# Performance work log

Hardware: AMD Instinct MI355X
Metric: run time of the kernel (lower is better)

The kernel has to match this reference:

```python
import jax, jax.numpy as jnp
import numpy as np

N, E, L, H, C, F, NCLASS, NGRAPH = 50000, 800000, 3, 2, 64, 128, 10, 64
NEG_SLOPE = 0.2


def setup_inputs() -> dict:
    key = jax.random.key(0)
    ks = jax.random.split(key, 8)
    x = jax.random.normal(ks[0], (N, F), dtype=jnp.float32)
    edge_index = jax.random.randint(ks[1], (2, E), 0, N, dtype=jnp.int64)
    batch = jnp.sort(jax.random.randint(ks[2], (N,), 0, NGRAPH, dtype=jnp.int64))
    s = 1.0 / np.sqrt(F)
    W = jax.random.normal(ks[3], (L, F, H * C), dtype=jnp.float32) * s
    att_src = jax.random.normal(ks[4], (L, H, C), dtype=jnp.float32) * s
    att_dst = jax.random.normal(ks[5], (L, H, C), dtype=jnp.float32) * s
    bias = jnp.zeros((L, H * C), dtype=jnp.float32)
    lin_w = jax.random.normal(ks[6], (H * C, NCLASS), dtype=jnp.float32) * s
    lin_b = jnp.zeros((NCLASS,), dtype=jnp.float32)
    return {"x": x, "edge_index": edge_index, "batch": batch, "W": W,
            "att_src": att_src, "att_dst": att_dst, "bias": bias,
            "lin_w": lin_w, "lin_b": lin_b}


def _gat_layer(x, src, dst, w, a_s, a_d, b):
    n = x.shape[0]
    h = (x @ w).reshape(n, H, C)                      # [N,H,C]
    alpha_src = jnp.sum(h * a_s, axis=-1)             # [N,H]
    alpha_dst = jnp.sum(h * a_d, axis=-1)             # [N,H]
    e = jax.nn.leaky_relu(alpha_src[src] + alpha_dst[dst], NEG_SLOPE)  # [E2,H]
    # scatter-softmax over incoming edges of each destination node
    m = jax.ops.segment_max(e, dst, num_segments=n)
    p = jnp.exp(e - m[dst])
    z = jax.ops.segment_sum(p, dst, num_segments=n)
    alpha = p / z[dst]                                # [E2,H]
    msg = h[src] * alpha[:, :, None]                  # [E2,H,C]
    out = jax.ops.segment_sum(msg, dst, num_segments=n)  # [N,H,C]
    return out.reshape(n, H * C) + b


def reference(x, edge_index, batch, W, att_src, att_dst, bias, lin_w, lin_b):
    n = x.shape[0]
    # PyG GATConv default: add self-loops
    loop = jnp.arange(n, dtype=edge_index.dtype)
    src = jnp.concatenate([edge_index[0], loop])
    dst = jnp.concatenate([edge_index[1], loop])
    for l in range(L):
        x = _gat_layer(x, src, dst, W[l], att_src[l], att_dst[l], bias[l])
        x = jax.nn.elu(x)  # activation; dropout/bn inactive (eval, use_bn=False)
    # global mean pool per graph
    sums = jax.ops.segment_sum(x, batch, num_segments=NGRAPH)
    cnt = jax.ops.segment_sum(jnp.ones((n,), x.dtype), batch, num_segments=NGRAPH)
    pooled = sums / jnp.maximum(cnt, 1.0)[:, None]    # [NGRAPH, H*C]
    logits = pooled @ lin_w + lin_b
    return jax.nn.softmax(logits, axis=1)
```

## Files before the change

kernel.cpp:

```cpp
#include <hip/hip_runtime.h>
#include <math.h>

#define NNODES 50000
#define NEDGES 800000
#define NLAYERS 3
#define NHEADS 2
#define NCH 64
#define FDIM 128
#define NCLS 10
#define NGRAPH 64
#define NEG_SLOPE 0.2f
#define GEMMB ((NNODES + 127) / 128)
#define NB 391
#define RADB 391
#define PCH 8

#define WAVE_SYNC()                      \
  do {                                   \
    __builtin_amdgcn_wave_barrier();     \
    __asm__ volatile("" ::: "memory");   \
  } while (0)

typedef __attribute__((ext_vector_type(8))) short bf16x8;
typedef __attribute__((ext_vector_type(4))) float f32x4;

__device__ __forceinline__ unsigned short f2bf(float f) {
  unsigned int u = __builtin_bit_cast(unsigned int, f);
  unsigned int r = u + 0x7FFFu + ((u >> 16) & 1u);
  return (unsigned short)(r >> 16);
}
__device__ __forceinline__ float bflo(unsigned v) {
  return __builtin_bit_cast(float, v << 16);
}
__device__ __forceinline__ float bfhi(unsigned v) {
  return __builtin_bit_cast(float, v & 0xFFFF0000u);
}

__global__ __launch_bounds__(256) void k_wprep(const float* __restrict__ W,
                                               unsigned* __restrict__ Wt,
                                               const int* __restrict__ batch,
                                               int* __restrict__ goff,
                                               float* __restrict__ gsum,
                                               int* __restrict__ bcnt,
                                               int* __restrict__ done) {
  __shared__ float Lt[128][132];
  int l = blockIdx.x;
  int t = threadIdx.x;
  if (l == NLAYERS) {
    if (t < NGRAPH) {
      int lo = 0, hi = NNODES;
      while (lo < hi) {
        int mid = (lo + hi) >> 1;
        if (batch[mid] < t) lo = mid + 1;
        else hi = mid;
      }
      goff[t] = lo;
    }
    if (t == 0) {
      goff[NGRAPH] = NNODES;
      *done = 0;
    }
    for (int i = t; i < NGRAPH * FDIM; i += 256) gsum[i] = 0.f;
    for (int i = t; i < NB; i += 256) bcnt[i] = 0;
    return;
  }
  const float* Wl = W + (size_t)l * FDIM * FDIM;
  unsigned* Wtl = Wt + (size_t)l * FDIM * FDIM / 2;
#pragma unroll
  for (int i = 0; i < 16; ++i) {
    int k = (t >> 5) + 8 * i;
    int n4 = (t & 31) * 4;
    float4 v = *(const float4*)(Wl + (size_t)k * 128 + n4);
    Lt[k][n4 + 0] = v.x;
    Lt[k][n4 + 1] = v.y;
    Lt[k][n4 + 2] = v.z;
    Lt[k][n4 + 3] = v.w;
  }
  __syncthreads();
  int n = t >> 1;
  int kh = (t & 1) * 64;
  for (int kk = 0; kk < 64; kk += 2) {
    unsigned pk = (unsigned)f2bf(Lt[kh + kk][n]) |
                  ((unsigned)f2bf(Lt[kh + kk + 1][n]) << 16);
    Wtl[n * 64 + (kh >> 1) + (kk >> 1)] = pk;
  }
}

template <bool BF16IN>
__device__ __forceinline__ void gemm_body(int blk, const void* __restrict__ Xv,
                                          const unsigned* __restrict__ Wt,
                                          const float* __restrict__ a_sL,
                                          const float* __restrict__ a_dL,
                                          unsigned* __restrict__ Hb,
                                          float* __restrict__ as_,
                                          float* __restrict__ ad_) {
  int t = threadIdx.x;
  int lane = t & 63;
  int w = t >> 6;
  int n16 = lane & 15;
  int quad = lane >> 4;
  int rowb = blk * 128 + w * 32;

  size_t rb[2];
  rb[0] = (size_t)min(rowb + n16, NNODES - 1) * 128;
  rb[1] = (size_t)min(rowb + 16 + n16, NNODES - 1) * 128;

  f32x4 acc[2][8];
#pragma unroll
  for (int mt = 0; mt < 2; ++mt)
#pragma unroll
    for (int nt = 0; nt < 8; ++nt) {
      f32x4 z = {0.f, 0.f, 0.f, 0.f};
      acc[mt][nt] = z;
    }
#pragma unroll
  for (int kk = 0; kk < 4; ++kk) {
    bf16x8 af[2];
#pragma unroll
    for (int mt = 0; mt < 2; ++mt) {
      if constexpr (BF16IN) {
        const unsigned short* xp = (const unsigned short*)Xv + rb[mt];
        af[mt] = *(const bf16x8*)(xp + kk * 32 + quad * 8);
      } else {
        const float* xp = (const float*)Xv + rb[mt];
        float4 va = *(const float4*)(xp + kk * 32 + quad * 8);
        float4 vb = *(const float4*)(xp + kk * 32 + quad * 8 + 4);
        af[mt][0] = (short)f2bf(va.x); af[mt][1] = (short)f2bf(va.y);
        af[mt][2] = (short)f2bf(va.z); af[mt][3] = (short)f2bf(va.w);
        af[mt][4] = (short)f2bf(vb.x); af[mt][5] = (short)f2bf(vb.y);
        af[mt][6] = (short)f2bf(vb.z); af[mt][7] = (short)f2bf(vb.w);
      }
    }
#pragma unroll
    for (int nt = 0; nt < 8; ++nt) {
      bf16x8 bf = *(const bf16x8*)(Wt + (size_t)(nt * 16 + n16) * 64 +
                                   kk * 16 + quad * 4);
      acc[0][nt] =
          __builtin_amdgcn_mfma_f32_16x16x32_bf16(af[0], bf, acc[0][nt], 0, 0, 0);
      acc[1][nt] =
          __builtin_amdgcn_mfma_f32_16x16x32_bf16(af[1], bf, acc[1][nt], 0, 0, 0);
    }
  }

  float asv[8], adv[8];
#pragma unroll
  for (int nt = 0; nt < 8; ++nt) {
    asv[nt] = a_sL[nt * 16 + n16];
    adv[nt] = a_dL[nt * 16 + n16];
  }
#pragma unroll
  for (int mt = 0; mt < 2; ++mt) {
#pragma unroll
    for (int r = 0; r < 4; ++r) {
      int row = rowb + mt * 16 + quad * 4 + r;
      bool ok = (row < NNODES);
      float ps0 = 0.f, pd0 = 0.f, ps1 = 0.f, pd1 = 0.f;
#pragma unroll
      for (int nt = 0; nt < 4; ++nt) {
        ps0 += acc[mt][nt][r] * asv[nt];
        pd0 += acc[mt][nt][r] * adv[nt];
        ps1 += acc[mt][nt + 4][r] * asv[nt + 4];
        pd1 += acc[mt][nt + 4][r] * adv[nt + 4];
      }
#pragma unroll
      for (int off = 1; off < 16; off <<= 1) {
        ps0 += __shfl_xor(ps0, off, 64);
        pd0 += __shfl_xor(pd0, off, 64);
        ps1 += __shfl_xor(ps1, off, 64);
        pd1 += __shfl_xor(pd1, off, 64);
      }
      if (ok && n16 == 0) {
        as_[row * 2 + 0] = ps0;
        as_[row * 2 + 1] = ps1;
        ad_[row * 2 + 0] = pd0;
        ad_[row * 2 + 1] = pd1;
      }
      if (ok) {
#pragma unroll
        for (int nt = 0; nt < 4; ++nt) {
          unsigned pk = (unsigned)f2bf(acc[mt][nt][r]) |
                        ((unsigned)f2bf(acc[mt][nt + 4][r]) << 16);
          Hb[(size_t)row * 64 + nt * 16 + n16] = pk;
        }
      }
    }
  }
}

__global__ __launch_bounds__(256) void k_gemm(
    const unsigned short* __restrict__ Xh, const unsigned* __restrict__ Wt,
    const float* __restrict__ a_sL, const float* __restrict__ a_dL,
    unsigned* __restrict__ Hb, float* __restrict__ as_,
    float* __restrict__ ad_) {
  gemm_body<true>(blockIdx.x, Xh, Wt, a_sL, a_dL, Hb, as_, ad_);
}

__global__ __launch_bounds__(256) void k_front(
    const float* __restrict__ X, const unsigned* __restrict__ Wt,
    const float* __restrict__ a_sL, const float* __restrict__ a_dL,
    unsigned* __restrict__ Hb, float* __restrict__ as_,
    float* __restrict__ ad_, const int* __restrict__ ei, int* __restrict__ bh,
    int* __restrict__ bcnt) {
  int b = blockIdx.x;
  if (b < GEMMB) {
    gemm_body<false>(b, X, Wt, a_sL, a_dL, Hb, as_, ad_);
  } else {
    __shared__ int hist[NB];
    int blk = b - GEMMB;
    int t = threadIdx.x;
    for (int i = t; i < NB; i += 256) hist[i] = 0;
    __syncthreads();
    int e0 = blk * 2048;
#pragma unroll
    for (int i = 0; i < 8; ++i) {
      int e = e0 + i * 256 + t;
      if (e < NEDGES) atomicAdd(&hist[ei[NEDGES + e] >> 7], 1);
    }
    __syncthreads();
    for (int i = t; i < NB; i += 256) {
      int c = hist[i];
      int base = c ? atomicAdd(&bcnt[i], c) : 0;
      bh[i * RADB + blk] = base;
    }
  }
}

__global__ __launch_bounds__(256) void k_passB(const int* __restrict__ ei,
                                               const int* __restrict__ bcnt,
                                               const int* __restrict__ bh,
                                               unsigned* __restrict__ ebuf,
                                               int* __restrict__ bstart) {
  __shared__ int curs[NB];
  __shared__ int ps[256];
  int blk = blockIdx.x, t = threadIdx.x;
  int x0 = (2 * t < NB) ? bcnt[2 * t] : 0;
  int x1 = (2 * t + 1 < NB) ? bcnt[2 * t + 1] : 0;
  int pair = x0 + x1;
  ps[t] = pair;
  __syncthreads();
  for (int off = 1; off < 256; off <<= 1) {
    int v = (t >= off) ? ps[t - off] : 0;
    __syncthreads();
    ps[t] += v;
    __syncthreads();
  }
  int ex = ps[t] - pair;
  if (2 * t < NB) {
    curs[2 * t] = ex + bh[(2 * t) * RADB + blk];
    if (blk == 0) bstart[2 * t] = ex;
  }
  if (2 * t + 1 < NB) {
    curs[2 * t + 1] = ex + x0 + bh[(2 * t + 1) * RADB + blk];
    if (blk == 0) bstart[2 * t + 1] = ex + x0;
  }
  if (blk == 0 && t == 0) bstart[NB] = NEDGES;
  __syncthreads();
  int e0 = blk * 2048;
#pragma unroll
  for (int i = 0; i < 8; ++i) {
    int e = e0 + i * 256 + t;
    if (e < NEDGES) {
      int s = ei[e];
      int d = ei[NEDGES + e];
      int pos = atomicAdd(&curs[d >> 7], 1);
      ebuf[pos] = ((unsigned)s << 7) | (unsigned)(d & 127);
    }
  }
}

__global__ __launch_bounds__(256) void k_passC(const unsigned* __restrict__ ebuf,
                                               const int* __restrict__ bstart,
                                               int* __restrict__ row_ptr,
                                               int* __restrict__ csr) {
  __shared__ int deg[128];
  __shared__ int scn[128];
  int b = blockIdx.x, t = threadIdx.x;
  int node0 = b * 128;
  int nn = min(128, NNODES - node0);
  int estart = bstart[b];
  int eend = bstart[b + 1];
  if (t < 128) deg[t] = 0;
  __syncthreads();
  for (int e = estart + t; e < eend; e += 256)
    atomicAdd(&deg[ebuf[e] & 127], 1);
  __syncthreads();
  if (t < 128) scn[t] = (t < nn) ? deg[t] + 1 : 0;
  __syncthreads();
  for (int off = 1; off < 128; off <<= 1) {
    int v = (t < 128 && t >= off) ? scn[t - off] : 0;
    __syncthreads();
    if (t < 128) scn[t] += v;
    __syncthreads();
  }
  int base = estart + node0;
  if (t < nn) {
    int st = base + (t ? scn[t - 1] : 0);
    row_ptr[node0 + t] = st;
    csr[st] = node0 + t;
    deg[t] = st + 1;
  }
  if (b == 0 && t == 0) row_ptr[NNODES] = NEDGES + NNODES;
  __syncthreads();
  for (int e = estart + t; e < eend; e += 256) {
    unsigned v = ebuf[e];
    int pos = atomicAdd(&deg[v & 127], 1);
    csr[pos] = (int)(v >> 7);
  }
}

__global__ __launch_bounds__(256) void k_aggregate(
    const unsigned* __restrict__ Hb, const float* __restrict__ as_,
    const float* __restrict__ ad_, const int* __restrict__ row_ptr,
    const int* __restrict__ csr, const float* __restrict__ bias,
    float* __restrict__ Xout, unsigned short* __restrict__ XoutH) {
  __shared__ float2 wb[4][64];
  __shared__ int sb[4][64];
  int wv = threadIdx.x >> 6;
  int lane = threadIdx.x & 63;
  int node = blockIdx.x * 4 + wv;
  if (node >= NNODES) return;
  int rs = row_ptr[node], re = row_ptr[node + 1];
  float2 adv = *(const float2*)&ad_[node * 2];
  const unsigned* Hl = Hb + lane;

  float z0 = 0.f, z1 = 0.f, acc0 = 0.f, acc1 = 0.f;
  for (int base = rs; base < re; base += 64) {
    int j = base + lane;
    int s = 0;
    if (j < re) s = csr[j];
    sb[wv][lane] = s;
    WAVE_SYNC();
    unsigned va[8];
#pragma unroll
    for (int u = 0; u < 8; ++u) va[u] = Hl[(size_t)sb[wv][u] * 64];
    float p0 = 0.f, p1 = 0.f;
    if (j < re) {
      float2 asv = *(const float2*)&as_[s * 2];
      float e0 = asv.x + adv.x; e0 = (e0 > 0.f) ? e0 : NEG_SLOPE * e0;
      float e1 = asv.y + adv.y; e1 = (e1 > 0.f) ? e1 : NEG_SLOPE * e1;
      p0 = __expf(e0);
      p1 = __expf(e1);
    }
    z0 += p0;
    z1 += p1;
    wb[wv][lane] = make_float2(p0, p1);
    WAVE_SYNC();
    int cl = min(64, re - base);
    int cl8 = (cl + 7) & ~7;
    int jj = 8;
    for (; jj < cl8; jj += 8) {
      unsigned vb2[8];
#pragma unroll
      for (int u = 0; u < 8; ++u) vb2[u] = Hl[(size_t)sb[wv][jj + u] * 64];
#pragma unroll
      for (int u = 0; u < 8; ++u) {
        float2 w = wb[wv][jj - 8 + u];
        acc0 += w.x * bflo(va[u]);
        acc1 += w.y * bfhi(va[u]);
      }
#pragma unroll
      for (int u = 0; u < 8; ++u) va[u] = vb2[u];
    }
#pragma unroll
    for (int u = 0; u < 8; ++u) {
      float2 w = wb[wv][jj - 8 + u];
      acc0 += w.x * bflo(va[u]);
      acc1 += w.y * bfhi(va[u]);
    }
    WAVE_SYNC();
  }
#pragma unroll
  for (int off = 32; off > 0; off >>= 1) {
    z0 += __shfl_xor(z0, off, 64);
    z1 += __shfl_xor(z1, off, 64);
  }
  float o0 = acc0 / z0 + bias[lane];
  float o1 = acc1 / z1 + bias[64 + lane];
  o0 = (o0 > 0.f) ? o0 : expm1f(o0);
  o1 = (o1 > 0.f) ? o1 : expm1f(o1);
  if (XoutH) {
    XoutH[(size_t)node * 128 + lane] = f2bf(o0);
    XoutH[(size_t)node * 128 + 64 + lane] = f2bf(o1);
  } else {
    Xout[(size_t)node * 128 + lane] = o0;
    Xout[(size_t)node * 128 + 64 + lane] = o1;
  }
}

__global__ __launch_bounds__(256) void k_pool2(const float* __restrict__ Xf,
                                               const int* __restrict__ goff,
                                               float* __restrict__ gsum,
                                               int* __restrict__ done,
                                               const float* __restrict__ lw,
                                               const float* __restrict__ lb,
                                               float* __restrict__ out) {
  __shared__ float4 red[8][32];
  __shared__ float sg[NGRAPH * 132];
  __shared__ int lastflag;
  int b = blockIdx.x;
  int g = b >> 3, ch = b & 7;
  int t = threadIdx.x;
  int cq = t & 31;
  int rh = t >> 5;
  int s = goff[g], e = goff[g + 1];
  int len = e - s;
  int c0 = s + (len * ch) / PCH;
  int c1 = s + (len * (ch + 1)) / PCH;
  float4 acc = make_float4(0.f, 0.f, 0.f, 0.f);
  for (int n = c0 + rh; n < c1; n += 8) {
    float4 v = *(const float4*)&Xf[(size_t)n * 128 + cq * 4];
    acc.x += v.x; acc.y += v.y; acc.z += v.z; acc.w += v.w;
  }
  red[rh][cq] = *(float4*)&acc;
  __syncthreads();
  if (t < 128) {
    float sum = 0.f;
#pragma unroll
    for (int ph = 0; ph < 8; ++ph)
      sum += ((const float*)&red[ph][t >> 2])[t & 3];
    atomicAdd(&gsum[g * FDIM + t], sum);
  }
  __syncthreads();
  if (t == 0) {
    __threadfence();
    int prev = atomicAdd(done, 1);
    lastflag = (prev == NGRAPH * PCH - 1) ? 1 : 0;
  }
  __syncthreads();
  if (!lastflag) return;
  __threadfence();
  for (int i = t; i < NGRAPH * FDIM; i += 256)
    sg[(i >> 7) * 132 + (i & 127)] = gsum[i];
  __syncthreads();
  if (t < NGRAPH) {
    int g2 = t;
    float cnt = (float)(goff[g2 + 1] - goff[g2]);
    float inv = 1.f / fmaxf(cnt, 1.f);
    float lg[NCLS];
#pragma unroll
    for (int k = 0; k < NCLS; ++k) lg[k] = lb[k];
    for (int cc = 0; cc < FDIM; ++cc) {
      float pv = sg[g2 * 132 + cc] * inv;
#pragma unroll
      for (int k = 0; k < NCLS; ++k) lg[k] += pv * lw[cc * NCLS + k];
    }
    float mx = lg[0];
#pragma unroll
    for (int k = 1; k < NCLS; ++k) mx = fmaxf(mx, lg[k]);
    float ssum = 0.f;
#pragma unroll
    for (int k = 0; k < NCLS; ++k) {
      lg[k] = expf(lg[k] - mx);
      ssum += lg[k];
    }
    float invs = 1.f / ssum;
#pragma unroll
    for (int k = 0; k < NCLS; ++k) out[g2 * NCLS + k] = lg[k] * invs;
  }
}


extern "C" void kernel_launch(void* const* d_in, const int* in_sizes, int n_in,
                              void* d_out, int out_size, void* d_ws,
                              size_t ws_size, hipStream_t stream) {
  const float* x = (const float*)d_in[0];
  const int* ei = (const int*)d_in[1];
  const int* batch = (const int*)d_in[2];
  const float* W = (const float*)d_in[3];
  const float* a_s = (const float*)d_in[4];
  const float* a_d = (const float*)d_in[5];
  const float* bias = (const float*)d_in[6];
  const float* lw = (const float*)d_in[7];
  const float* lb = (const float*)d_in[8];
  float* out = (float*)d_out;

  unsigned* Hb = (unsigned*)d_ws;
  float* xb = (float*)(Hb + (size_t)NNODES * 64);
  float* as_ = xb + (size_t)NNODES * 128;
  float* ad_ = as_ + (size_t)NNODES * 2;
  float* gsum = ad_ + (size_t)NNODES * 2;
  int* goff = (int*)(gsum + NGRAPH * FDIM);
  int* bcnt = goff + (NGRAPH + 1);
  int* bstart = bcnt + NB;
  int* row_ptr = bstart + (NB + 1);
  int* csr = row_ptr + (NNODES + 1);
  int* bh = csr + (NEDGES + NNODES);
  unsigned* ebuf = (unsigned*)(bh + NB * RADB);
  unsigned* Wt = ebuf + (NEDGES + 1024);
  unsigned short* xbh = (unsigned short*)(Wt + 3 * 8192);
  int* done = (int*)(xbh + (size_t)NNODES * 128);

  k_wprep<<<NLAYERS + 1, 256, 0, stream>>>(W, Wt, batch, goff, gsum, bcnt,
                                           done);
  k_front<<<GEMMB + RADB, 256, 0, stream>>>(x, Wt, a_s, a_d, Hb, as_, ad_, ei,
                                            bh, bcnt);
  k_passB<<<RADB, 256, 0, stream>>>(ei, bcnt, bh, ebuf, bstart);
  k_passC<<<NB, 256, 0, stream>>>(ebuf, bstart, row_ptr, csr);

  for (int l = 0; l < NLAYERS; ++l) {
    if (l > 0) {
      k_gemm<<<GEMMB, 256, 0, stream>>>(xbh, Wt + (size_t)l * FDIM * FDIM / 2,
                                        a_s + l * FDIM, a_d + l * FDIM, Hb,
                                        as_, ad_);
    }
    unsigned short* oh = (l < NLAYERS - 1) ? xbh : nullptr;
    k_aggregate<<<(NNODES + 3) / 4, 256, 0, stream>>>(
        Hb, as_, ad_, row_ptr, csr, bias + l * FDIM, xb, oh);
  }
  k_pool2<<<NGRAPH * PCH, 256, 0, stream>>>(xb, goff, gsum, done, lw, lb, out);
}
```

Baseline: 290.7 us.

## Aggregate with 16 lanes per node using 128-bit row gathers

Restructures the GAT aggregation kernel so each destination node is handled by a 16-lane group instead of a full 64-lane wavefront. Each lane gathers a uint4 (four packed bf16 pairs) per neighbour row and accumulates eight channels, which widens memory transactions and stops wasting lanes on the short neighbour lists (average degree about 17). Row pointers are staged in shared memory, and outputs are written as vector stores. In exchange, each lane holds more registers and does more serial work per edge, and the reductions now run over 16-lane subgroups.

Measured after the change: 300.1 us. 1.03x slower.

```diff
diff --git a/kernel.cpp b/kernel.cpp
--- a/kernel.cpp
+++ b/kernel.cpp
@@ -313,26 +313,29 @@
     const float* __restrict__ ad_, const int* __restrict__ row_ptr,
     const int* __restrict__ csr, const float* __restrict__ bias,
     float* __restrict__ Xout, unsigned short* __restrict__ XoutH) {
-  __shared__ float2 wb[4][64];
-  __shared__ int sb[4][64];
-  int wv = threadIdx.x >> 6;
-  int lane = threadIdx.x & 63;
-  int node = blockIdx.x * 4 + wv;
-  if (node >= NNODES) return;
-  int rs = row_ptr[node], re = row_ptr[node + 1];
+  __shared__ int rp[17];
+  __shared__ int sb[16][16];
+  __shared__ float2 wb[16][16];
+  int t = threadIdx.x;
+  int ng = t >> 4;
+  int gl = t & 15;
+  int node0 = blockIdx.x * 16;
+  if (t < 17) rp[t] = row_ptr[node0 + t];
+  __syncthreads();
+  int node = node0 + ng;
+  int rs = rp[ng], re = rp[ng + 1];
   float2 adv = *(const float2*)&ad_[node * 2];
-  const unsigned* Hl = Hb + lane;
-
-  float z0 = 0.f, z1 = 0.f, acc0 = 0.f, acc1 = 0.f;
-  for (int base = rs; base < re; base += 64) {
-    int j = base + lane;
+  const uint4* Hq = (const uint4*)Hb;
+
+  float z0 = 0.f, z1 = 0.f;
+  float a00 = 0.f, a01 = 0.f, a02 = 0.f, a03 = 0.f;
+  float a10 = 0.f, a11 = 0.f, a12 = 0.f, a13 = 0.f;
+  for (int base = rs; base < re; base += 16) {
+    int j = base + gl;
     int s = 0;
     if (j < re) s = csr[j];
-    sb[wv][lane] = s;
+    sb[ng][gl] = s;
     WAVE_SYNC();
-    unsigned va[8];
-#pragma unroll
-    for (int u = 0; u < 8; ++u) va[u] = Hl[(size_t)sb[wv][u] * 64];
     float p0 = 0.f, p1 = 0.f;
     if (j < re) {
       float2 asv = *(const float2*)&as_[s * 2];
@@ -343,47 +346,68 @@
     }
     z0 += p0;
     z1 += p1;
-    wb[wv][lane] = make_float2(p0, p1);
+    wb[ng][gl] = make_float2(p0, p1);
     WAVE_SYNC();
-    int cl = min(64, re - base);
-    int cl8 = (cl + 7) & ~7;
-    int jj = 8;
-    for (; jj < cl8; jj += 8) {
-      unsigned vb2[8];
-#pragma unroll
-      for (int u = 0; u < 8; ++u) vb2[u] = Hl[(size_t)sb[wv][jj + u] * 64];
-#pragma unroll
-      for (int u = 0; u < 8; ++u) {
-        float2 w = wb[wv][jj - 8 + u];
-        acc0 += w.x * bflo(va[u]);
-        acc1 += w.y * bfhi(va[u]);
-      }
-#pragma unroll
-      for (int u = 0; u < 8; ++u) va[u] = vb2[u];
-    }
-#pragma unroll
-    for (int u = 0; u < 8; ++u) {
-      float2 w = wb[wv][jj - 8 + u];
-      acc0 += w.x * bflo(va[u]);
-      acc1 += w.y * bfhi(va[u]);
+    int cl = min(16, re - base);
+    int cl4 = (cl + 3) & ~3;
+    uint4 va[4];
+#pragma unroll
+    for (int u = 0; u < 4; ++u) va[u] = Hq[(size_t)sb[ng][u] * 16 + gl];
+    int jj = 4;
+    for (; jj < cl4; jj += 4) {
+      uint4 vb2[4];
+#pragma unroll
+      for (int u = 0; u < 4; ++u) vb2[u] = Hq[(size_t)sb[ng][jj + u] * 16 + gl];
+#pragma unroll
+      for (int u = 0; u < 4; ++u) {
+        float2 w = wb[ng][jj - 4 + u];
+        a00 += w.x * bflo(va[u].x); a10 += w.y * bfhi(va[u].x);
+        a01 += w.x * bflo(va[u].y); a11 += w.y * bfhi(va[u].y);
+        a02 += w.x * bflo(va[u].z); a12 += w.y * bfhi(va[u].z);
+        a03 += w.x * bflo(va[u].w); a13 += w.y * bfhi(va[u].w);
+      }
+#pragma unroll
+      for (int u = 0; u < 4; ++u) va[u] = vb2[u];
+    }
+#pragma unroll
+    for (int u = 0; u < 4; ++u) {
+      float2 w = wb[ng][jj - 4 + u];
+      a00 += w.x * bflo(va[u].x); a10 += w.y * bfhi(va[u].x);
+      a01 += w.x * bflo(va[u].y); a11 += w.y * bfhi(va[u].y);
+      a02 += w.x * bflo(va[u].z); a12 += w.y * bfhi(va[u].z);
+      a03 += w.x * bflo(va[u].w); a13 += w.y * bfhi(va[u].w);
     }
     WAVE_SYNC();
   }
 #pragma unroll
-  for (int off = 32; off > 0; off >>= 1) {
-    z0 += __shfl_xor(z0, off, 64);
-    z1 += __shfl_xor(z1, off, 64);
-  }
-  float o0 = acc0 / z0 + bias[lane];
-  float o1 = acc1 / z1 + bias[64 + lane];
-  o0 = (o0 > 0.f) ? o0 : expm1f(o0);
-  o1 = (o1 > 0.f) ? o1 : expm1f(o1);
+  for (int off = 1; off < 16; off <<= 1) {
+    z0 += __shfl_xor(z0, off, 16);
+    z1 += __shfl_xor(z1, off, 16);
+  }
+  float4 b0 = *(const float4*)&bias[gl * 4];
+  float4 b1 = *(const float4*)&bias[64 + gl * 4];
+  float o00 = a00 / z0 + b0.x, o01 = a01 / z0 + b0.y;
+  float o02 = a02 / z0 + b0.z, o03 = a03 / z0 + b0.w;
+  float o10 = a10 / z1 + b1.x, o11 = a11 / z1 + b1.y;
+  float o12 = a12 / z1 + b1.z, o13 = a13 / z1 + b1.w;
+  o00 = (o00 > 0.f) ? o00 : expm1f(o00);
+  o01 = (o01 > 0.f) ? o01 : expm1f(o01);
+  o02 = (o02 > 0.f) ? o02 : expm1f(o02);
+  o03 = (o03 > 0.f) ? o03 : expm1f(o03);
+  o10 = (o10 > 0.f) ? o10 : expm1f(o10);
+  o11 = (o11 > 0.f) ? o11 : expm1f(o11);
+  o12 = (o12 > 0.f) ? o12 : expm1f(o12);
+  o13 = (o13 > 0.f) ? o13 : expm1f(o13);
   if (XoutH) {
-    XoutH[(size_t)node * 128 + lane] = f2bf(o0);
-    XoutH[(size_t)node * 128 + 64 + lane] = f2bf(o1);
+    ushort4 h0 = make_ushort4(f2bf(o00), f2bf(o01), f2bf(o02), f2bf(o03));
+    ushort4 h1 = make_ushort4(f2bf(o10), f2bf(o11), f2bf(o12), f2bf(o13));
+    *(ushort4*)&XoutH[(size_t)node * 128 + gl * 4] = h0;
+    *(ushort4*)&XoutH[(size_t)node * 128 + 64 + gl * 4] = h1;
   } else {
-    Xout[(size_t)node * 128 + lane] = o0;
-    Xout[(size_t)node * 128 + 64 + lane] = o1;
+    *(float4*)&Xout[(size_t)node * 128 + gl * 4] =
+        make_float4(o00, o01, o02, o03);
+    *(float4*)&Xout[(size_t)node * 128 + 64 + gl * 4] =
+        make_float4(o10, o11, o12, o13);
   }
 }
 
@@ -504,7 +528,7 @@
                                         as_, ad_);
     }
     unsigned short* oh = (l < NLAYERS - 1) ? xbh : nullptr;
-    k_aggregate<<<(NNODES + 3) / 4, 256, 0, stream>>>(
+    k_aggregate<<<(NNODES + 15) / 16, 256, 0, stream>>>(
         Hb, as_, ad_, row_ptr, csr, bias + l * FDIM, xb, oh);
   }
   k_pool2<<<NGRAPH * PCH, 256, 0, stream>>>(xb, goff, gsum, done, lw, lb, out);
```
